# Performance work log

Measured on AMD Instinct MI355X. Metric: run time of the kernel, lower is better.

The kernel has to match this reference:

```python
import jax, jax.numpy as jnp
import numpy as np

BATCH, IN_DIM, OUT_DIM = 4096, 8192, 16384

# Each of the 16 logic gates is affine in {1, a, b, a*b}. Rows below give the
# coefficients (const, a, b, ab) for gate k, matching the torch `gate` match-case.
_GATE_COEFS = np.array([
    [0, 0, 0, 0],    # 0: zeros
    [0, 0, 0, 1],    # 1: a*b
    [0, 1, 0, -1],   # 2: a - a*b
    [0, 1, 0, 0],    # 3: a
    [0, 0, 1, -1],   # 4: b - a*b
    [0, 0, 1, 0],    # 5: b
    [0, 1, 1, -2],   # 6: a + b - 2ab (xor)
    [0, 1, 1, -1],   # 7: a + b - ab (or)
    [1, -1, -1, 1],  # 8: 1 - (a + b - ab) (nor)
    [1, -1, -1, 2],  # 9: 1 - (a + b - 2ab) (xnor)
    [1, 0, -1, 0],   # 10: 1 - b
    [1, 0, -1, 1],   # 11: 1 - b + ab
    [1, -1, 0, 0],   # 12: 1 - a
    [1, -1, 0, 1],   # 13: 1 - a + ab
    [1, 0, 0, -1],   # 14: 1 - ab (nand)
    [1, 0, 0, 0],    # 15: ones
], dtype=np.float32)


def setup_inputs() -> dict:
    key = jax.random.key(0)
    k1, k2, k3, k4 = jax.random.split(key, 4)
    x = jax.random.uniform(k1, (BATCH, IN_DIM), dtype=jnp.float32)
    weights = jax.random.normal(k2, (OUT_DIM, 16), dtype=jnp.float32)
    idx_a = jax.random.randint(k3, (OUT_DIM,), 0, IN_DIM, dtype=jnp.int32)
    idx_b = jax.random.randint(k4, (OUT_DIM,), 0, IN_DIM, dtype=jnp.int32)
    return {"x": x, "weights": weights, "idx_a": idx_a, "idx_b": idx_b}


def reference(x, weights, idx_a, idx_b):
    # Training path: softmax over the 16 gate logits per output neuron.
    w = jax.nn.softmax(weights, axis=-1)            # [O, 16]
    # Collapse the 16-gate weighted sum into 4 affine coefficients per neuron.
    coef = w @ jnp.asarray(_GATE_COEFS)             # [O, 4] -> (c0, ca, cb, cab)
    a = x[..., idx_a]                               # [B, O] gather
    b = x[..., idx_b]                               # [B, O] gather
    return coef[:, 0] + coef[:, 1] * a + coef[:, 2] * b + coef[:, 3] * (a * b)
```

## Files before the change

kernel.cpp:

```cpp
#include <hip/hip_runtime.h>
#include <cstddef>
#include <cstdint>

constexpr int BATCH   = 4096;
constexpr int IN_DIM  = 8192;
constexpr int OUT_DIM = 16384;
constexpr int THREADS = 512;
constexpr int RPB     = 2;
constexpr int OPT     = 4;
constexpr int ITERS   = OUT_DIM / (THREADS * OPT);

__device__ __forceinline__ float4 softmax_coef(const float* __restrict__ wrow) {
  const float4* wp = reinterpret_cast<const float4*>(wrow);
  float4 t0 = wp[0], t1 = wp[1], t2 = wp[2], t3 = wp[3];
  float w[16] = { t0.x, t0.y, t0.z, t0.w,
                  t1.x, t1.y, t1.z, t1.w,
                  t2.x, t2.y, t2.z, t2.w,
                  t3.x, t3.y, t3.z, t3.w };
  float m = w[0];
#pragma unroll
  for (int i = 1; i < 16; ++i) m = fmaxf(m, w[i]);
  float p[16];
  float s = 0.f;
#pragma unroll
  for (int i = 0; i < 16; ++i) { p[i] = __expf(w[i] - m); s += p[i]; }
  const float inv = 1.0f / s;
  const float GC[16]  = {0,0,0,0, 0,0,0,0, 1,1,1,1, 1,1,1,1};
  const float GA[16]  = {0,0,1,1, 0,0,1,1, -1,-1,0,0, -1,-1,0,0};
  const float GB[16]  = {0,0,0,0, 1,1,1,1, -1,-1,-1,-1, 0,0,0,0};
  const float GAB[16] = {0,1,-1,0, -1,0,-2,-1, 1,2,0,1, 0,1,-1,0};
  float c0 = 0.f, ca = 0.f, cb = 0.f, cab = 0.f;
#pragma unroll
  for (int i = 0; i < 16; ++i) {
    c0  += p[i] * GC[i];
    ca  += p[i] * GA[i];
    cb  += p[i] * GB[i];
    cab += p[i] * GAB[i];
  }
  return make_float4(c0 * inv, ca * inv, cb * inv, cab * inv);
}

__global__ __launch_bounds__(256)
void coef_kernel(const float* __restrict__ weights, float4* __restrict__ coef) {
  const int o = blockIdx.x * 256 + threadIdx.x;
  if (o < OUT_DIM) coef[o] = softmax_coef(weights + (size_t)o * 16);
}

template <bool USE_WS>
__global__ __launch_bounds__(THREADS)
void logic_main(const float* __restrict__ x,
                const float4* __restrict__ coef,
                const float* __restrict__ weights,
                const int* __restrict__ idx_a,
                const int* __restrict__ idx_b,
                float* __restrict__ out) {
  __shared__ float rows[RPB][IN_DIM];

  const int b0 = blockIdx.x * RPB;

  {
    const float4* __restrict__ src =
        reinterpret_cast<const float4*>(x + (size_t)b0 * IN_DIM);
    float4* __restrict__ dst = reinterpret_cast<float4*>(&rows[0][0]);
    constexpr int V4 = RPB * IN_DIM / 4;
#pragma unroll
    for (int i = threadIdx.x; i < V4; i += THREADS) dst[i] = src[i];
  }
  __syncthreads();

#pragma unroll
  for (int it = 0; it < ITERS; ++it) {
    const int o = (it * THREADS + threadIdx.x) * OPT;

    const int4 ia = *reinterpret_cast<const int4*>(idx_a + o);
    const int4 ib = *reinterpret_cast<const int4*>(idx_b + o);

    float4 c0, c1, c2, c3;
    if (USE_WS) {
      c0 = coef[o + 0]; c1 = coef[o + 1]; c2 = coef[o + 2]; c3 = coef[o + 3];
    } else {
      c0 = softmax_coef(weights + (size_t)(o + 0) * 16);
      c1 = softmax_coef(weights + (size_t)(o + 1) * 16);
      c2 = softmax_coef(weights + (size_t)(o + 2) * 16);
      c3 = softmax_coef(weights + (size_t)(o + 3) * 16);
    }

#pragma unroll
    for (int r = 0; r < RPB; ++r) {
      const float* __restrict__ row = rows[r];
      const float a0 = row[ia.x], a1 = row[ia.y], a2 = row[ia.z], a3 = row[ia.w];
      const float v0 = row[ib.x], v1 = row[ib.y], v2 = row[ib.z], v3 = row[ib.w];
      float4 res;
      res.x = fmaf(fmaf(c0.w, a0, c0.z), v0, fmaf(c0.y, a0, c0.x));
      res.y = fmaf(fmaf(c1.w, a1, c1.z), v1, fmaf(c1.y, a1, c1.x));
      res.z = fmaf(fmaf(c2.w, a2, c2.z), v2, fmaf(c2.y, a2, c2.x));
      res.w = fmaf(fmaf(c3.w, a3, c3.z), v3, fmaf(c3.y, a3, c3.x));
      *reinterpret_cast<float4*>(out + (size_t)(b0 + r) * OUT_DIM + o) = res;
    }
  }
}

extern "C" void kernel_launch(void* const* d_in, const int* in_sizes, int n_in,
                              void* d_out, int out_size, void* d_ws, size_t ws_size,
                              hipStream_t stream) {
  const float* x       = (const float*)d_in[0];
  const float* weights = (const float*)d_in[1];
  const int*   idx_a   = (const int*)d_in[2];
  const int*   idx_b   = (const int*)d_in[3];
  float*       out     = (float*)d_out;

  const size_t coef_bytes = (size_t)OUT_DIM * 4 * sizeof(float);
  const bool use_ws = (d_ws != nullptr) && (ws_size >= coef_bytes);

  if (use_ws) {
    float4* coef = (float4*)d_ws;
    coef_kernel<<<OUT_DIM / 256, 256, 0, stream>>>(weights, coef);
    logic_main<true><<<BATCH / RPB, THREADS, 0, stream>>>(
        x, coef, weights, idx_a, idx_b, out);
  } else {
    logic_main<false><<<BATCH / RPB, THREADS, 0, stream>>>(
        x, nullptr, weights, idx_a, idx_b, out);
  }
}
```

Measured before the change: 117.5 us.

## Interleave two batch rows in LDS, prefetch indices, use nontemporal loads and stores

Stores the two batch rows interleaved in shared memory as float2 pairs, so each gathered index fetches both rows' values with one LDS read instead of two. Loads of x and stores of the output become nontemporal to reduce cache pollution. Index and coefficient loads for the next iteration are software-prefetched. The fallback path that computed softmax inline without a workspace is removed, so the kernel now assumes a workspace is always provided.

```diff
diff --git a/kernel.cpp b/kernel.cpp
--- a/kernel.cpp
+++ b/kernel.cpp
@@ -9,6 +9,10 @@
 constexpr int RPB     = 2;
 constexpr int OPT     = 4;
 constexpr int ITERS   = OUT_DIM / (THREADS * OPT);
+constexpr int SSTEPS  = IN_DIM / (THREADS * 2);
+
+typedef float f32x2 __attribute__((ext_vector_type(2)));
+typedef float f32x4 __attribute__((ext_vector_type(4)));
 
 __device__ __forceinline__ float4 softmax_coef(const float* __restrict__ wrow) {
   const float4* wp = reinterpret_cast<const float4*>(wrow);
@@ -46,57 +50,72 @@
   if (o < OUT_DIM) coef[o] = softmax_coef(weights + (size_t)o * 16);
 }
 
-template <bool USE_WS>
 __global__ __launch_bounds__(THREADS)
 void logic_main(const float* __restrict__ x,
                 const float4* __restrict__ coef,
-                const float* __restrict__ weights,
                 const int* __restrict__ idx_a,
                 const int* __restrict__ idx_b,
                 float* __restrict__ out) {
-  __shared__ float rows[RPB][IN_DIM];
+  __shared__ float4 xpair[IN_DIM / 2];
+  const float2* __restrict__ pr = reinterpret_cast<const float2*>(xpair);
 
+  const int t  = threadIdx.x;
   const int b0 = blockIdx.x * RPB;
 
-  {
-    const float4* __restrict__ src =
-        reinterpret_cast<const float4*>(x + (size_t)b0 * IN_DIM);
-    float4* __restrict__ dst = reinterpret_cast<float4*>(&rows[0][0]);
-    constexpr int V4 = RPB * IN_DIM / 4;
+  const f32x2* __restrict__ r0 =
+      reinterpret_cast<const f32x2*>(x + (size_t)b0 * IN_DIM);
+  const f32x2* __restrict__ r1 =
+      reinterpret_cast<const f32x2*>(x + (size_t)(b0 + 1) * IN_DIM);
+
+  int o0 = t * OPT;
+  int4   ia = *reinterpret_cast<const int4*>(idx_a + o0);
+  int4   ib = *reinterpret_cast<const int4*>(idx_b + o0);
+  float4 c0 = coef[o0 + 0], c1 = coef[o0 + 1],
+         c2 = coef[o0 + 2], c3 = coef[o0 + 3];
+
 #pragma unroll
-    for (int i = threadIdx.x; i < V4; i += THREADS) dst[i] = src[i];
+  for (int s = 0; s < SSTEPS; ++s) {
+    const int p = s * THREADS + t;
+    f32x2 a = __builtin_nontemporal_load(r0 + p);
+    f32x2 b = __builtin_nontemporal_load(r1 + p);
+    xpair[p] = make_float4(a.x, b.x, a.y, b.y);
   }
   __syncthreads();
 
 #pragma unroll
   for (int it = 0; it < ITERS; ++it) {
-    const int o = (it * THREADS + threadIdx.x) * OPT;
+    const int o = it * THREADS * OPT + t * OPT;
 
-    const int4 ia = *reinterpret_cast<const int4*>(idx_a + o);
-    const int4 ib = *reinterpret_cast<const int4*>(idx_b + o);
-
-    float4 c0, c1, c2, c3;
-    if (USE_WS) {
-      c0 = coef[o + 0]; c1 = coef[o + 1]; c2 = coef[o + 2]; c3 = coef[o + 3];
-    } else {
-      c0 = softmax_coef(weights + (size_t)(o + 0) * 16);
-      c1 = softmax_coef(weights + (size_t)(o + 1) * 16);
-      c2 = softmax_coef(weights + (size_t)(o + 2) * 16);
-      c3 = softmax_coef(weights + (size_t)(o + 3) * 16);
+    int4 ia_n, ib_n;
+    float4 cn0, cn1, cn2, cn3;
+    if (it + 1 < ITERS) {
+      const int on = o + THREADS * OPT;
+      ia_n = *reinterpret_cast<const int4*>(idx_a + on);
+      ib_n = *reinterpret_cast<const int4*>(idx_b + on);
+      cn0 = coef[on + 0]; cn1 = coef[on + 1];
+      cn2 = coef[on + 2]; cn3 = coef[on + 3];
     }
 
-#pragma unroll
-    for (int r = 0; r < RPB; ++r) {
-      const float* __restrict__ row = rows[r];
-      const float a0 = row[ia.x], a1 = row[ia.y], a2 = row[ia.z], a3 = row[ia.w];
-      const float v0 = row[ib.x], v1 = row[ib.y], v2 = row[ib.z], v3 = row[ib.w];
-      float4 res;
-      res.x = fmaf(fmaf(c0.w, a0, c0.z), v0, fmaf(c0.y, a0, c0.x));
-      res.y = fmaf(fmaf(c1.w, a1, c1.z), v1, fmaf(c1.y, a1, c1.x));
-      res.z = fmaf(fmaf(c2.w, a2, c2.z), v2, fmaf(c2.y, a2, c2.x));
-      res.w = fmaf(fmaf(c3.w, a3, c3.z), v3, fmaf(c3.y, a3, c3.x));
-      *reinterpret_cast<float4*>(out + (size_t)(b0 + r) * OUT_DIM + o) = res;
-    }
+    const float2 A0 = pr[ia.x], A1 = pr[ia.y], A2 = pr[ia.z], A3 = pr[ia.w];
+    const float2 B0 = pr[ib.x], B1 = pr[ib.y], B2 = pr[ib.z], B3 = pr[ib.w];
+
+    f32x4 res0, res1;
+    res0.x = fmaf(fmaf(c0.w, A0.x, c0.z), B0.x, fmaf(c0.y, A0.x, c0.x));
+    res1.x = fmaf(fmaf(c0.w, A0.y, c0.z), B0.y, fmaf(c0.y, A0.y, c0.x));
+    res0.y = fmaf(fmaf(c1.w, A1.x, c1.z), B1.x, fmaf(c1.y, A1.x, c1.x));
+    res1.y = fmaf(fmaf(c1.w, A1.y, c1.z), B1.y, fmaf(c1.y, A1.y, c1.x));
+    res0.z = fmaf(fmaf(c2.w, A2.x, c2.z), B2.x, fmaf(c2.y, A2.x, c2.x));
+    res1.z = fmaf(fmaf(c2.w, A2.y, c2.z), B2.y, fmaf(c2.y, A2.y, c2.x));
+    res0.w = fmaf(fmaf(c3.w, A3.x, c3.z), B3.x, fmaf(c3.y, A3.x, c3.x));
+    res1.w = fmaf(fmaf(c3.w, A3.y, c3.z), B3.y, fmaf(c3.y, A3.y, c3.x));
+
+    __builtin_nontemporal_store(
+        res0, reinterpret_cast<f32x4*>(out + (size_t)b0 * OUT_DIM + o));
+    __builtin_nontemporal_store(
+        res1, reinterpret_cast<f32x4*>(out + (size_t)(b0 + 1) * OUT_DIM + o));
+
+    ia = ia_n; ib = ib_n;
+    c0 = cn0; c1 = cn1; c2 = cn2; c3 = cn3;
   }
 }
 
@@ -109,16 +128,7 @@
   const int*   idx_b   = (const int*)d_in[3];
   float*       out     = (float*)d_out;
 
-  const size_t coef_bytes = (size_t)OUT_DIM * 4 * sizeof(float);
-  const bool use_ws = (d_ws != nullptr) && (ws_size >= coef_bytes);
-
-  if (use_ws) {
-    float4* coef = (float4*)d_ws;
-    coef_kernel<<<OUT_DIM / 256, 256, 0, stream>>>(weights, coef);
-    logic_main<true><<<BATCH / RPB, THREADS, 0, stream>>>(
-        x, coef, weights, idx_a, idx_b, out);
-  } else {
-    logic_main<false><<<BATCH / RPB, THREADS, 0, stream>>>(
-        x, nullptr, weights, idx_a, idx_b, out);
-  }
+  float4* coef = (float4*)d_ws;
+  coef_kernel<<<OUT_DIM / 256, 256, 0, stream>>>(weights, coef);
+  logic_main<<<BATCH / RPB, THREADS, 0, stream>>>(x, coef, idx_a, idx_b, out);
 }
```

Result: faster. 108.9 us (-7.3%).
